# Performance work log

Hardware: AMD Instinct MI355X
Metric: run time of the kernel (lower is better)

The kernel has to match this reference:

```python
import jax, jax.numpy as jnp
import numpy as np

N = 384          # item_num (text regions)
TD = 768         # text hidden (bert-base)
VD = 768         # vision hidden (vit-base)
CD = TD + VD     # commu_dim = 1536
FF = 2048        # TransformerEncoderLayer default dim_feedforward
H = 4            # nhead
L = 2            # num_layers per encoder
EPS = 1e-5


def _enc_params(key, d, scale=0.02):
    ks = jax.random.split(key, 6)
    return dict(
        qkv_w=jax.random.normal(ks[0], (L, 3 * d, d), jnp.float32) * scale,
        qkv_b=jnp.zeros((L, 3 * d), jnp.float32),
        out_w=jax.random.normal(ks[1], (L, d, d), jnp.float32) * scale,
        out_b=jnp.zeros((L, d), jnp.float32),
        ln1_s=jnp.ones((L, d), jnp.float32),
        ln1_b=jnp.zeros((L, d), jnp.float32),
        ff1_w=jax.random.normal(ks[2], (L, FF, d), jnp.float32) * scale,
        ff1_b=jnp.zeros((L, FF), jnp.float32),
        ff2_w=jax.random.normal(ks[3], (L, d, FF), jnp.float32) * scale,
        ff2_b=jnp.zeros((L, d), jnp.float32),
        ln2_s=jnp.ones((L, d), jnp.float32),
        ln2_b=jnp.zeros((L, d), jnp.float32),
    )


def setup_inputs() -> dict:
    key = jax.random.key(0)
    k = jax.random.split(key, 6)
    inp = {
        'text_emb': jax.random.normal(k[0], (N, TD), jnp.float32),
        'vision_emb': jax.random.normal(k[1], (N, VD), jnp.float32),
        'gt_matrix': jax.random.randint(k[2], (N, N), 0, 2, jnp.int32),
    }
    for pref, kk, d in (('t_', k[3], TD), ('c_', k[4], CD)):
        for name, v in _enc_params(kk, d).items():
            inp[pref + name] = v
    inp['lin_w'] = jax.random.normal(k[5], (2, 2 * CD), jnp.float32) * 0.02
    inp['lin_b'] = jnp.zeros((2,), jnp.float32)
    return inp


def _ln(x, s, b):
    m = jnp.mean(x, -1, keepdims=True)
    v = jnp.mean((x - m) ** 2, -1, keepdims=True)
    return (x - m) * jax.lax.rsqrt(v + EPS) * s + b


def _encoder(x, qkv_w, qkv_b, out_w, out_b, ln1_s, ln1_b,
             ff1_w, ff1_b, ff2_w, ff2_b, ln2_s, ln2_b):
    # PyTorch post-norm TransformerEncoder, relu activation, eval mode (no dropout)
    d = x.shape[-1]
    hd = d // H
    for l in range(qkv_w.shape[0]):
        qkv = x @ qkv_w[l].T + qkv_b[l]
        q, kk, v = jnp.split(qkv, 3, axis=-1)
        q = q.reshape(-1, H, hd)
        kk = kk.reshape(-1, H, hd)
        v = v.reshape(-1, H, hd)
        scores = jnp.einsum('qhd,khd->hqk', q, kk) / jnp.sqrt(jnp.float32(hd))
        attn = jax.nn.softmax(scores, -1)
        o = jnp.einsum('hqk,khd->qhd', attn, v).reshape(-1, d)
        x = _ln(x + o @ out_w[l].T + out_b[l], ln1_s[l], ln1_b[l])
        h = jax.nn.relu(x @ ff1_w[l].T + ff1_b[l]) @ ff2_w[l].T + ff2_b[l]
        x = _ln(x + h, ln2_s[l], ln2_b[l])
    return x


def reference(text_emb, vision_emb, gt_matrix,
              t_qkv_w, t_qkv_b, t_out_w, t_out_b, t_ln1_s, t_ln1_b,
              t_ff1_w, t_ff1_b, t_ff2_w, t_ff2_b, t_ln2_s, t_ln2_b,
              c_qkv_w, c_qkv_b, c_out_w, c_out_b, c_ln1_s, c_ln1_b,
              c_ff1_w, c_ff1_b, c_ff2_w, c_ff2_b, c_ln2_s, c_ln2_b,
              lin_w, lin_b):
    te = _encoder(text_emb, t_qkv_w, t_qkv_b, t_out_w, t_out_b, t_ln1_s, t_ln1_b,
                  t_ff1_w, t_ff1_b, t_ff2_w, t_ff2_b, t_ln2_s, t_ln2_b)
    all_emb = jnp.concatenate([te, vision_emb], axis=1)  # [N, CD]
    all_emb = _encoder(all_emb, c_qkv_w, c_qkv_b, c_out_w, c_out_b, c_ln1_s, c_ln1_b,
                       c_ff1_w, c_ff1_b, c_ff2_w, c_ff2_b, c_ln2_s, c_ln2_b)
    # organize(): linear(cat(e_i, e_j)) decomposes exactly as e_i@Wa^T + e_j@Wb^T + b,
    # avoiding the O(N^2 * 2*CD) pair tensor while computing identical math.
    a = all_emb @ lin_w[:, :CD].T + lin_b      # [N, 2]
    c = all_emb @ lin_w[:, CD:].T              # [N, 2]
    logits = a[:, None, :] + c[None, :, :]     # [N, N, 2]
    probs = jax.nn.softmax(logits, -1)         # self.activate(self.linear(...))
    # classificaiton_loss: sum_i CrossEntropyLoss(probs[i], gt[i])  (CE takes probs as logits)
    ls = jax.nn.log_softmax(probs, -1)
    cell = -jnp.take_along_axis(ls, gt_matrix[..., None].astype(jnp.int32), axis=-1)[..., 0]
    cls_loss = jnp.sum(jnp.mean(cell, axis=1))
    # enter_exit_loss over first N-1 items
    link = probs[:, :, 1]
    ee_loss = jnp.sum(jnp.abs(link.sum(1)[:-1] + link.sum(0)[:-1] - 1.0))
    return probs, cls_loss, ee_loss
```

## Files before the change

kernel.cpp:

```cpp
#include <hip/hip_runtime.h>
#include <hip/hip_bf16.h>
#include <math.h>

#define NTOK 384
#define HEADS 4

typedef __attribute__((ext_vector_type(8))) short bf16x8;
typedef __attribute__((ext_vector_type(4))) float f32x4;

__device__ __forceinline__ unsigned short f2b(float f) {
    union { float f; unsigned int u; } v; v.f = f;
    unsigned int r = (v.u + 0x7fff + ((v.u >> 16) & 1)) >> 16;
    return (unsigned short)r;
}

__device__ __forceinline__ void g2l16(const void* g, void* l) {
    __builtin_amdgcn_global_load_lds(
        (const __attribute__((address_space(1))) unsigned int*)g,
        (__attribute__((address_space(3))) unsigned int*)l, 16, 0, 0);
}

__device__ __forceinline__ void stage64(
    const unsigned short* __restrict__ g, int row0, int k0, int ld,
    char* region, int wid, int lane)
{
    int c = wid * 64 + lane;
    int row = c >> 2, p = c & 3;
    int kc = (p - (row >> 1)) & 3;
    g2l16(g + (long)(row0 + row) * ld + k0 + kc * 8,
          region + (wid * 64) * 16);
}

__device__ __forceinline__ void stage_tile(
    const unsigned short* __restrict__ A, const unsigned short* __restrict__ B,
    int row0, int col0, int k0, int lda, int ldb,
    char* buf, int wid, int lane)
{
    stage64(A, row0, k0,      lda, buf,         wid, lane);
    stage64(A, row0, k0 + 32, lda, buf +  4096, wid, lane);
    stage64(B, col0, k0,      ldb, buf +  8192, wid, lane);
    stage64(B, col0, k0 + 32, ldb, buf + 12288, wid, lane);
    __builtin_amdgcn_sched_barrier(0);
}

__global__ __launch_bounds__(256, 3) void gemm64(
    const unsigned short* __restrict__ A, const unsigned short* __restrict__ B,
    const float* __restrict__ bias, void* __restrict__ Cv,
    int K, int lda, int ldb, int ldc,
    long sA, long sB, long sC, int relu, int out_bf16,
    unsigned short* __restrict__ vt, int dv2)
{
    __shared__ char smem[3][16384];
    A += (long)blockIdx.z * sA;
    B += (long)blockIdx.z * sB;
    const int t = threadIdx.x, lane = t & 63, wid = t >> 6;
    const int wm = wid >> 1, wn = wid & 1;
    const int r16 = lane & 15, quad = lane >> 4;
    const int row0 = blockIdx.y * 64, col0 = blockIdx.x * 64;

    f32x4 acc[2][2] = {};
    const int NT = K >> 6;

    stage_tile(A, B, row0, col0, 0, lda, ldb, smem[0], wid, lane);
    if (NT > 1)
        stage_tile(A, B, row0, col0, 64, lda, ldb, smem[1], wid, lane);

    int cur = 0, sb = 2;
    for (int kt = 0; kt < NT; ++kt) {
        if (kt + 1 < NT) asm volatile("s_waitcnt vmcnt(4)" ::: "memory");
        else             asm volatile("s_waitcnt vmcnt(0) lgkmcnt(0)" ::: "memory");
        __builtin_amdgcn_s_barrier();
        if (kt + 2 < NT) {
            stage_tile(A, B, row0, col0, (kt + 2) * 64, lda, ldb,
                       smem[sb], wid, lane);
            sb = (sb == 2) ? 0 : sb + 1;
        }
        const char* cb = smem[cur];
        cur = (cur == 2) ? 0 : cur + 1;
        #pragma unroll
        for (int h = 0; h < 2; ++h) {
            bf16x8 af[2], bfv[2];
            #pragma unroll
            for (int rt = 0; rt < 2; ++rt) {
                int row = wm * 32 + rt * 16 + r16;
                int p = (quad + (row >> 1)) & 3;
                af[rt] = *reinterpret_cast<const bf16x8*>(
                    cb + h * 4096 + row * 64 + p * 16);
            }
            #pragma unroll
            for (int ct = 0; ct < 2; ++ct) {
                int col = wn * 32 + ct * 16 + r16;
                int p = (quad + (col >> 1)) & 3;
                bfv[ct] = *reinterpret_cast<const bf16x8*>(
                    cb + 8192 + h * 4096 + col * 64 + p * 16);
            }
            #pragma unroll
            for (int rt = 0; rt < 2; ++rt)
                #pragma unroll
                for (int ct = 0; ct < 2; ++ct)
                    acc[rt][ct] = __builtin_amdgcn_mfma_f32_16x16x32_bf16(
                        af[rt], bfv[ct], acc[rt][ct], 0, 0, 0);
        }
    }

    float* Cf = (float*)Cv;
    unsigned short* Cb = (unsigned short*)Cv;
    const long zoff = (long)blockIdx.z * sC;
    const int vwrite = (vt != nullptr) && (col0 >= dv2);
    #pragma unroll
    for (int rt = 0; rt < 2; ++rt) {
        #pragma unroll
        for (int ct = 0; ct < 2; ++ct) {
            f32x4 v = acc[rt][ct];
            int col = col0 + wn * 32 + ct * 16 + r16;
            float bi = bias ? bias[col] : 0.f;
            #pragma unroll
            for (int i = 0; i < 4; ++i) {
                v[i] += bi;
                if (relu) v[i] = fmaxf(v[i], 0.f);
            }
            int rbase = row0 + wm * 32 + rt * 16 + quad * 4;
            if (vwrite) {
                ushort4 p;
                p.x = f2b(v[0]); p.y = f2b(v[1]); p.z = f2b(v[2]); p.w = f2b(v[3]);
                *reinterpret_cast<ushort4*>(vt + (long)(col - dv2) * NTOK + rbase) = p;
            } else if (out_bf16) {
                #pragma unroll
                for (int i = 0; i < 4; ++i)
                    Cb[zoff + (long)(rbase + i) * ldc + col] = f2b(v[i]);
            } else {
                #pragma unroll
                for (int i = 0; i < 4; ++i)
                    Cf[zoff + (long)(rbase + i) * ldc + col] = v[i];
            }
        }
    }
}

#define WO0 0u
#define WO1 3538944u
#define WO2 4718592u
#define WO3 7864320u
#define WO4 11010048u
#define WO5 25165824u
#define WO6 29884416u
#define WO7 36175872u
#define WTOT 42467328u

__global__ __launch_bounds__(256) void convert_weights(
    const float* __restrict__ s0, const float* __restrict__ s1,
    const float* __restrict__ s2, const float* __restrict__ s3,
    const float* __restrict__ s4, const float* __restrict__ s5,
    const float* __restrict__ s6, const float* __restrict__ s7,
    unsigned short* __restrict__ dst)
{
    unsigned int e = (blockIdx.x * 256u + threadIdx.x) * 16u;
    if (e >= WTOT) return;
    const float* src; unsigned int local;
    if      (e < WO1) { src = s0; local = e - WO0; }
    else if (e < WO2) { src = s1; local = e - WO1; }
    else if (e < WO3) { src = s2; local = e - WO2; }
    else if (e < WO4) { src = s3; local = e - WO3; }
    else if (e < WO5) { src = s4; local = e - WO4; }
    else if (e < WO6) { src = s5; local = e - WO5; }
    else if (e < WO7) { src = s6; local = e - WO6; }
    else              { src = s7; local = e - WO7; }
    float4 v0 = *reinterpret_cast<const float4*>(src + local);
    float4 v1 = *reinterpret_cast<const float4*>(src + local + 4);
    float4 v2 = *reinterpret_cast<const float4*>(src + local + 8);
    float4 v3 = *reinterpret_cast<const float4*>(src + local + 12);
    uint4 o0, o1;
    o0.x = (unsigned)f2b(v0.x) | ((unsigned)f2b(v0.y) << 16);
    o0.y = (unsigned)f2b(v0.z) | ((unsigned)f2b(v0.w) << 16);
    o0.z = (unsigned)f2b(v1.x) | ((unsigned)f2b(v1.y) << 16);
    o0.w = (unsigned)f2b(v1.z) | ((unsigned)f2b(v1.w) << 16);
    o1.x = (unsigned)f2b(v2.x) | ((unsigned)f2b(v2.y) << 16);
    o1.y = (unsigned)f2b(v2.z) | ((unsigned)f2b(v2.w) << 16);
    o1.z = (unsigned)f2b(v3.x) | ((unsigned)f2b(v3.y) << 16);
    o1.w = (unsigned)f2b(v3.z) | ((unsigned)f2b(v3.w) << 16);
    *reinterpret_cast<uint4*>(dst + e) = o0;
    *reinterpret_cast<uint4*>(dst + e + 8) = o1;
}

__global__ __launch_bounds__(64) void softmax_rows(
    const float* __restrict__ S, unsigned short* __restrict__ P, float scale)
{
    const float* p = S + (long)blockIdx.x * NTOK;
    unsigned short* q = P + (long)blockIdx.x * NTOK;
    const int t = threadIdx.x;
    float vals[6];
    float vmax = -1e30f;
    #pragma unroll
    for (int i = 0; i < 6; ++i) {
        vals[i] = p[t + i * 64] * scale;
        vmax = fmaxf(vmax, vals[i]);
    }
    for (int off = 32; off; off >>= 1) vmax = fmaxf(vmax, __shfl_down(vmax, off));
    vmax = __shfl(vmax, 0);
    float sum = 0.f;
    #pragma unroll
    for (int i = 0; i < 6; ++i) { vals[i] = __expf(vals[i] - vmax); sum += vals[i]; }
    for (int off = 32; off; off >>= 1) sum += __shfl_down(sum, off);
    sum = __shfl(sum, 0);
    float inv = 1.f / sum;
    #pragma unroll
    for (int i = 0; i < 6; ++i) q[t + i * 64] = f2b(vals[i] * inv);
}

__global__ __launch_bounds__(256) void add_ln(
    float* __restrict__ x, unsigned short* __restrict__ xb,
    const float* __restrict__ y, long ps, int np,
    const float* __restrict__ gb,
    const float* __restrict__ s, const float* __restrict__ b, int d)
{
    float* xr = x + (long)blockIdx.x * d;
    unsigned short* xbr = xb + (long)blockIdx.x * d;
    const float* yr = y + (long)blockIdx.x * d;
    const int t = threadIdx.x;
    float vv[6];
    float s1 = 0.f, s2 = 0.f;
    #pragma unroll
    for (int j = 0; j < 6; ++j) {
        int i = t + j * 256;
        if (j * 256 < d) {
            float v = xr[i] + gb[i];
            for (int p = 0; p < np; ++p) v += yr[i + p * ps];
            vv[j] = v;
            s1 += v; s2 += v * v;
        }
    }
    for (int off = 32; off; off >>= 1) { s1 += __shfl_down(s1, off); s2 += __shfl_down(s2, off); }
    __shared__ float r1[4], r2[4];
    int w = t >> 6;
    if ((t & 63) == 0) { r1[w] = s1; r2[w] = s2; }
    __syncthreads();
    if (t == 0) {
        float a = 0.f, c = 0.f;
        for (int i = 0; i < 4; ++i) { a += r1[i]; c += r2[i]; }
        r1[0] = a; r2[0] = c;
    }
    __syncthreads();
    float mean = r1[0] / d;
    float var = r2[0] / d - mean * mean;
    float rstd = rsqrtf(var + 1e-5f);
    #pragma unroll
    for (int j = 0; j < 6; ++j) {
        int i = t + j * 256;
        if (j * 256 < d) {
            float v = (vv[j] - mean) * rstd * s[i] + b[i];
            xr[i] = v;
            xbr[i] = f2b(v);
        }
    }
}

__global__ void initx_k(const float* __restrict__ src, float* __restrict__ dst,
                        unsigned short* __restrict__ dstb, int n)
{
    int i = blockIdx.x * blockDim.x + threadIdx.x;
    if (i < n) { float v = src[i]; dst[i] = v; dstb[i] = f2b(v); }
}

__global__ void concat_k(const float* __restrict__ te, const float* __restrict__ ve,
                         float* __restrict__ all, unsigned short* __restrict__ allb)
{
    int i = blockIdx.x * blockDim.x + threadIdx.x;
    if (i >= NTOK * 1536) return;
    int r = i / 1536, c = i % 1536;
    float v = (c < 768) ? te[r * 768 + c] : ve[r * 768 + (c - 768)];
    all[i] = v;
    allb[i] = f2b(v);
}

__global__ __launch_bounds__(256) void head_ac(
    const float* __restrict__ all, const float* __restrict__ lin_w,
    const float* __restrict__ lin_b, float* __restrict__ a, float* __restrict__ c)
{
    const int i = blockIdx.x, t = threadIdx.x;
    const float* xr = all + (long)i * 1536;
    float s0 = 0.f, s1 = 0.f, s2 = 0.f, s3 = 0.f;
    for (int e = t; e < 1536; e += 256) {
        float v = xr[e];
        s0 += v * lin_w[e];
        s1 += v * lin_w[3072 + e];
        s2 += v * lin_w[1536 + e];
        s3 += v * lin_w[4608 + e];
    }
    for (int off = 32; off; off >>= 1) {
        s0 += __shfl_down(s0, off); s1 += __shfl_down(s1, off);
        s2 += __shfl_down(s2, off); s3 += __shfl_down(s3, off);
    }
    __shared__ float r[4][4];
    int w = t >> 6;
    if ((t & 63) == 0) { r[0][w] = s0; r[1][w] = s1; r[2][w] = s2; r[3][w] = s3; }
    __syncthreads();
    if (t == 0) {
        float t0 = 0.f, t1 = 0.f, t2 = 0.f, t3 = 0.f;
        for (int k = 0; k < 4; ++k) { t0 += r[0][k]; t1 += r[1][k]; t2 += r[2][k]; t3 += r[3][k]; }
        a[i * 2 + 0] = t0 + lin_b[0];
        a[i * 2 + 1] = t1 + lin_b[1];
        c[i * 2 + 0] = t2;
        c[i * 2 + 1] = t3;
    }
}

__global__ __launch_bounds__(384) void head_probs(
    const float* __restrict__ a, const float* __restrict__ c,
    const int* __restrict__ gt, float* __restrict__ probs,
    float* __restrict__ rowsum, float* __restrict__ rowcell)
{
    const int i = blockIdx.x, j = threadIdx.x;
    float l0 = a[i * 2 + 0] + c[j * 2 + 0];
    float l1 = a[i * 2 + 1] + c[j * 2 + 1];
    float m = fmaxf(l0, l1);
    float e0 = __expf(l0 - m), e1 = __expf(l1 - m);
    float inv = 1.f / (e0 + e1);
    float p0 = e0 * inv, p1 = e1 * inv;
    long base = ((long)i * NTOK + j) * 2;
    probs[base] = p0;
    probs[base + 1] = p1;
    float m2 = fmaxf(p0, p1);
    float z = m2 + __logf(__expf(p0 - m2) + __expf(p1 - m2));
    int g = gt[i * NTOK + j];
    float cell = z - (g ? p1 : p0);
    float cs = cell, ps = p1;
    for (int off = 32; off; off >>= 1) { cs += __shfl_down(cs, off); ps += __shfl_down(ps, off); }
    __shared__ float rc[6], rs[6];
    int w = j >> 6;
    if ((j & 63) == 0) { rc[w] = cs; rs[w] = ps; }
    __syncthreads();
    if (j == 0) {
        float csum = 0.f, psum = 0.f;
        for (int k = 0; k < 6; ++k) { csum += rc[k]; psum += rs[k]; }
        rowcell[i] = csum * (1.f / NTOK);
        rowsum[i] = psum;
    }
}

__global__ __launch_bounds__(64) void colsum_k(const float* __restrict__ probs,
                                               float* __restrict__ colsum)
{
    const int j = blockIdx.x, t = threadIdx.x;
    float s = 0.f;
    for (int i = t; i < NTOK; i += 64)
        s += probs[((long)i * NTOK + j) * 2 + 1];
    for (int off = 32; off; off >>= 1) s += __shfl_down(s, off);
    if (t == 0) colsum[j] = s;
}

__global__ __launch_bounds__(384) void finalize_k(
    const float* __restrict__ rowcell, const float* __restrict__ rowsum,
    const float* __restrict__ colsum, float* __restrict__ out)
{
    const int t = threadIdx.x;
    float cls = rowcell[t];
    float ee = (t < NTOK - 1) ? fabsf(rowsum[t] + colsum[t] - 1.f) : 0.f;
    for (int off = 32; off; off >>= 1) { cls += __shfl_down(cls, off); ee += __shfl_down(ee, off); }
    __shared__ float rc[6], re[6];
    int w = t >> 6;
    if ((t & 63) == 0) { rc[w] = cls; re[w] = ee; }
    __syncthreads();
    if (t == 0) {
        float a = 0.f, b = 0.f;
        for (int k = 0; k < 6; ++k) { a += rc[k]; b += re[k]; }
        out[NTOK * NTOK * 2 + 0] = a;
        out[NTOK * NTOK * 2 + 1] = b;
    }
}

static void run_encoder(float* x, unsigned short* xb, int d,
                        const unsigned short* wq, const unsigned short* wo,
                        const unsigned short* w1, const unsigned short* w2,
                        const float* qkv_b, const float* out_b,
                        const float* ln1_s, const float* ln1_b,
                        const float* ff1_b, const float* ff2_b,
                        const float* ln2_s, const float* ln2_b,
                        unsigned short* qkvb, float* sc, unsigned short* attnb,
                        unsigned short* vtb, unsigned short* ob,
                        unsigned short* t1b, float* t2,
                        hipStream_t stream)
{
    const int dq = 3 * d;
    const int hd = d / HEADS;
    const float scale = 1.0f / sqrtf((float)hd);
    const int np_out = (d == 768) ? 2 : 3;
    const int ks_out = d / np_out;
    const int np_ff2 = 4, ks_ff2 = 512;
    const long psC = (long)NTOK * d;
    for (int l = 0; l < 2; ++l) {
        gemm64<<<dim3(dq / 64, 6), 256, 0, stream>>>(
            xb, wq + (long)l * dq * d, qkv_b + l * dq, qkvb,
            d, d, d, dq, 0, 0, 0, 0, 1, vtb, 2 * d);
        gemm64<<<dim3(6, 6, HEADS), 256, 0, stream>>>(
            qkvb, qkvb + d, nullptr, sc,
            hd, dq, dq, NTOK, (long)hd, (long)hd, (long)NTOK * NTOK,
            0, 0, nullptr, 0);
        softmax_rows<<<HEADS * NTOK, 64, 0, stream>>>(sc, attnb, scale);
        gemm64<<<dim3(hd / 64, 6, HEADS), 256, 0, stream>>>(
            attnb, vtb, nullptr, ob,
            NTOK, NTOK, NTOK, d, (long)NTOK * NTOK, (long)hd * NTOK, (long)hd,
            0, 1, nullptr, 0);
        gemm64<<<dim3(d / 64, 6, np_out), 256, 0, stream>>>(
            ob, wo + (long)l * d * d, nullptr, t2,
            ks_out, d, d, d, (long)ks_out, (long)ks_out, psC, 0, 0, nullptr, 0);
        add_ln<<<NTOK, 256, 0, stream>>>(x, xb, t2, psC, np_out,
                                         out_b + l * d, ln1_s + l * d, ln1_b + l * d, d);
        gemm64<<<dim3(2048 / 64, 6), 256, 0, stream>>>(
            xb, w1 + (long)l * 2048 * d, ff1_b + l * 2048, t1b,
            d, d, d, 2048, 0, 0, 0, 1, 1, nullptr, 0);
        gemm64<<<dim3(d / 64, 6, np_ff2), 256, 0, stream>>>(
            t1b, w2 + (long)l * d * 2048, nullptr, t2,
            ks_ff2, 2048, 2048, d, (long)ks_ff2, (long)ks_ff2, psC, 0, 0, nullptr, 0);
        add_ln<<<NTOK, 256, 0, stream>>>(x, xb, t2, psC, np_ff2,
                                         ff2_b + l * d, ln2_s + l * d, ln2_b + l * d, d);
    }
}

extern "C" void kernel_launch(void* const* d_in, const int* in_sizes, int n_in,
                              void* d_out, int out_size, void* d_ws, size_t ws_size,
                              hipStream_t stream)
{
    const float* text_emb   = (const float*)d_in[0];
    const float* vision_emb = (const float*)d_in[1];
    const int*   gt         = (const int*)  d_in[2];
    const float* t_qkv_w = (const float*)d_in[3];
    const float* t_qkv_b = (const float*)d_in[4];
    const float* t_out_w = (const float*)d_in[5];
    const float* t_out_b = (const float*)d_in[6];
    const float* t_ln1_s = (const float*)d_in[7];
    const float* t_ln1_b = (const float*)d_in[8];
    const float* t_ff1_w = (const float*)d_in[9];
    const float* t_ff1_b = (const float*)d_in[10];
    const float* t_ff2_w = (const float*)d_in[11];
    const float* t_ff2_b = (const float*)d_in[12];
    const float* t_ln2_s = (const float*)d_in[13];
    const float* t_ln2_b = (const float*)d_in[14];
    const float* c_qkv_w = (const float*)d_in[15];
    const float* c_qkv_b = (const float*)d_in[16];
    const float* c_out_w = (const float*)d_in[17];
    const float* c_out_b = (const float*)d_in[18];
    const float* c_ln1_s = (const float*)d_in[19];
    const float* c_ln1_b = (const float*)d_in[20];
    const float* c_ff1_w = (const float*)d_in[21];
    const float* c_ff1_b = (const float*)d_in[22];
    const float* c_ff2_w = (const float*)d_in[23];
    const float* c_ff2_b = (const float*)d_in[24];
    const float* c_ln2_s = (const float*)d_in[25];
    const float* c_ln2_b = (const float*)d_in[26];
    const float* lin_w   = (const float*)d_in[27];
    const float* lin_b   = (const float*)d_in[28];
    float* out = (float*)d_out;

    float* ws = (float*)d_ws;
    float* xt      = ws;
    float* all     = xt + 294912;
    float* t2      = all + 589824;
    float* sc      = t2 + 2359296;
    float* abuf    = sc + 589824;
    float* cbuf    = abuf + 768;
    float* rowsum  = cbuf + 768;
    float* rowcell = rowsum + 384;
    float* colsum  = rowcell + 384;
    unsigned short* ub = (unsigned short*)(ws + 3836544);
    unsigned short* xtb   = ub;
    unsigned short* allb  = xtb + 294912;
    unsigned short* qkvb  = allb + 589824;
    unsigned short* attnb = qkvb + 1769472;
    unsigned short* vtb   = attnb + 589824;
    unsigned short* ob    = vtb + 589824;
    unsigned short* t1b   = ob + 589824;
    unsigned short* wb    = t1b + 786432;

    convert_weights<<<(WTOT / 16 + 255) / 256, 256, 0, stream>>>(
        t_qkv_w, t_out_w, t_ff1_w, t_ff2_w,
        c_qkv_w, c_out_w, c_ff1_w, c_ff2_w, wb);

    initx_k<<<(294912 + 255) / 256, 256, 0, stream>>>(text_emb, xt, xtb, 294912);
    run_encoder(xt, xtb, 768,
                wb + WO0, wb + WO1, wb + WO2, wb + WO3,
                t_qkv_b, t_out_b, t_ln1_s, t_ln1_b,
                t_ff1_b, t_ff2_b, t_ln2_s, t_ln2_b,
                qkvb, sc, attnb, vtb, ob, t1b, t2, stream);

    concat_k<<<(589824 + 255) / 256, 256, 0, stream>>>(xt, vision_emb, all, allb);
    run_encoder(all, allb, 1536,
                wb + WO4, wb + WO5, wb + WO6, wb + WO7,
                c_qkv_b, c_out_b, c_ln1_s, c_ln1_b,
                c_ff1_b, c_ff2_b, c_ln2_s, c_ln2_b,
                qkvb, sc, attnb, vtb, ob, t1b, t2, stream);

    head_ac<<<NTOK, 256, 0, stream>>>(all, lin_w, lin_b, abuf, cbuf);
    head_probs<<<NTOK, 384, 0, stream>>>(abuf, cbuf, gt, out, rowsum, rowcell);
    colsum_k<<<NTOK, 64, 0, stream>>>(out, colsum);
    finalize_k<<<1, 384, 0, stream>>>(rowcell, rowsum, colsum, out);
}
```

Measured before the change: 514.4 us.

## Use 128x128 GEMM tiles for projections and drop split-K partial sums

Adds a 512-thread gemm128 kernel with 128x128 output tiles and uses it for the QKV, output-projection, FF1 and FF2 GEMMs. The output-projection and FF2 GEMMs no longer split K into partial slabs, so add_ln reads a single result instead of summing partials, and the workspace layout shrinks to match. Larger tiles raise per-block data reuse and cut partial-sum traffic, but they launch far fewer blocks (for example 6x3 for the d=768 projections), which can leave most of the GPU's compute units idle and make each block run the full K loop.

```diff
diff --git a/kernel.cpp b/kernel.cpp
--- a/kernel.cpp
+++ b/kernel.cpp
@@ -47,8 +47,7 @@
     const unsigned short* __restrict__ A, const unsigned short* __restrict__ B,
     const float* __restrict__ bias, void* __restrict__ Cv,
     int K, int lda, int ldb, int ldc,
-    long sA, long sB, long sC, int relu, int out_bf16,
-    unsigned short* __restrict__ vt, int dv2)
+    long sA, long sB, long sC, int relu, int out_bf16)
 {
     __shared__ char smem[3][16384];
     A += (long)blockIdx.z * sA;
@@ -106,7 +105,6 @@
     float* Cf = (float*)Cv;
     unsigned short* Cb = (unsigned short*)Cv;
     const long zoff = (long)blockIdx.z * sC;
-    const int vwrite = (vt != nullptr) && (col0 >= dv2);
     #pragma unroll
     for (int rt = 0; rt < 2; ++rt) {
         #pragma unroll
@@ -120,6 +118,114 @@
                 if (relu) v[i] = fmaxf(v[i], 0.f);
             }
             int rbase = row0 + wm * 32 + rt * 16 + quad * 4;
+            if (out_bf16) {
+                #pragma unroll
+                for (int i = 0; i < 4; ++i)
+                    Cb[zoff + (long)(rbase + i) * ldc + col] = f2b(v[i]);
+            } else {
+                #pragma unroll
+                for (int i = 0; i < 4; ++i)
+                    Cf[zoff + (long)(rbase + i) * ldc + col] = v[i];
+            }
+        }
+    }
+}
+
+__device__ __forceinline__ void stage128(
+    const unsigned short* __restrict__ g, int row0, int k0, int ld,
+    char* region, int tid)
+{
+    int row = tid >> 2, p = tid & 3;
+    int kc = (p - (row >> 1)) & 3;
+    g2l16(g + (long)(row0 + row) * ld + k0 + kc * 8,
+          region + ((tid >> 6) * 64) * 16);
+}
+
+__device__ __forceinline__ void stage_tile128(
+    const unsigned short* __restrict__ A, const unsigned short* __restrict__ B,
+    int row0, int col0, int k0, int lda, int ldb,
+    char* buf, int tid)
+{
+    stage128(A, row0, k0,      lda, buf,          tid);
+    stage128(A, row0, k0 + 32, lda, buf +  8192,  tid);
+    stage128(B, col0, k0,      ldb, buf + 16384,  tid);
+    stage128(B, col0, k0 + 32, ldb, buf + 24576,  tid);
+    __builtin_amdgcn_sched_barrier(0);
+}
+
+__global__ __launch_bounds__(512, 1) void gemm128(
+    const unsigned short* __restrict__ A, const unsigned short* __restrict__ B,
+    const float* __restrict__ bias, void* __restrict__ Cv,
+    int K, int lda, int ldb, int ldc, int relu, int out_bf16,
+    unsigned short* __restrict__ vt, int dv2)
+{
+    __shared__ char smem[3][32768];
+    const int t = threadIdx.x, lane = t & 63, wid = t >> 6;
+    const int wm = wid >> 2, wn = wid & 3;
+    const int r16 = lane & 15, quad = lane >> 4;
+    const int row0 = blockIdx.y * 128, col0 = blockIdx.x * 128;
+
+    f32x4 acc[4][2] = {};
+    const int NT = K >> 6;
+
+    stage_tile128(A, B, row0, col0, 0, lda, ldb, smem[0], t);
+    if (NT > 1)
+        stage_tile128(A, B, row0, col0, 64, lda, ldb, smem[1], t);
+
+    int cur = 0, sb = 2;
+    for (int kt = 0; kt < NT; ++kt) {
+        if (kt + 1 < NT) asm volatile("s_waitcnt vmcnt(4)" ::: "memory");
+        else             asm volatile("s_waitcnt vmcnt(0) lgkmcnt(0)" ::: "memory");
+        __builtin_amdgcn_s_barrier();
+        if (kt + 2 < NT) {
+            stage_tile128(A, B, row0, col0, (kt + 2) * 64, lda, ldb,
+                          smem[sb], t);
+            sb = (sb == 2) ? 0 : sb + 1;
+        }
+        const char* cb = smem[cur];
+        cur = (cur == 2) ? 0 : cur + 1;
+        #pragma unroll
+        for (int h = 0; h < 2; ++h) {
+            bf16x8 af[4], bfv[2];
+            #pragma unroll
+            for (int rt = 0; rt < 4; ++rt) {
+                int row = wm * 64 + rt * 16 + r16;
+                int p = (quad + (row >> 1)) & 3;
+                af[rt] = *reinterpret_cast<const bf16x8*>(
+                    cb + h * 8192 + row * 64 + p * 16);
+            }
+            #pragma unroll
+            for (int ct = 0; ct < 2; ++ct) {
+                int col = wn * 32 + ct * 16 + r16;
+                int p = (quad + (col >> 1)) & 3;
+                bfv[ct] = *reinterpret_cast<const bf16x8*>(
+                    cb + 16384 + h * 8192 + col * 64 + p * 16);
+            }
+            #pragma unroll
+            for (int rt = 0; rt < 4; ++rt)
+                #pragma unroll
+                for (int ct = 0; ct < 2; ++ct)
+                    acc[rt][ct] = __builtin_amdgcn_mfma_f32_16x16x32_bf16(
+                        af[rt], bfv[ct], acc[rt][ct], 0, 0, 0);
+        }
+    }
+
+    float* Cf = (float*)Cv;
+    unsigned short* Cb = (unsigned short*)Cv;
+    const int vwrite = (vt != nullptr) && (col0 >= dv2);
+    #pragma unroll
+    for (int rt = 0; rt < 4; ++rt) {
+        #pragma unroll
+        for (int ct = 0; ct < 2; ++ct) {
+            f32x4 v = acc[rt][ct];
+            int col = col0 + wn * 32 + ct * 16 + r16;
+            float bi = bias ? bias[col] : 0.f;
+            #pragma unroll
+            for (int i = 0; i < 4; ++i) {
+                v[i] += bi;
+                if (relu) v[i] = fmaxf(v[i], 0.f);
+            }
+            int rbase = row0 + wm * 64 + rt * 16 + quad * 4;
             if (vwrite) {
                 ushort4 p;
                 p.x = f2b(v[0]); p.y = f2b(v[1]); p.z = f2b(v[2]); p.w = f2b(v[3]);
@@ -127,11 +233,11 @@
             } else if (out_bf16) {
                 #pragma unroll
                 for (int i = 0; i < 4; ++i)
-                    Cb[zoff + (long)(rbase + i) * ldc + col] = f2b(v[i]);
+                    Cb[(long)(rbase + i) * ldc + col] = f2b(v[i]);
             } else {
                 #pragma unroll
                 for (int i = 0; i < 4; ++i)
-                    Cf[zoff + (long)(rbase + i) * ldc + col] = v[i];
+                    Cf[(long)(rbase + i) * ldc + col] = v[i];
             }
         }
     }
@@ -209,7 +315,7 @@
 
 __global__ __launch_bounds__(256) void add_ln(
     float* __restrict__ x, unsigned short* __restrict__ xb,
-    const float* __restrict__ y, long ps, int np,
+    const float* __restrict__ y,
     const float* __restrict__ gb,
     const float* __restrict__ s, const float* __restrict__ b, int d)
 {
@@ -223,8 +329,7 @@
     for (int j = 0; j < 6; ++j) {
         int i = t + j * 256;
         if (j * 256 < d) {
-            float v = xr[i] + gb[i];
-            for (int p = 0; p < np; ++p) v += yr[i + p * ps];
+            float v = xr[i] + gb[i] + yr[i];
             vv[j] = v;
             s1 += v; s2 += v * v;
         }
@@ -383,35 +488,30 @@
     const int dq = 3 * d;
     const int hd = d / HEADS;
     const float scale = 1.0f / sqrtf((float)hd);
-    const int np_out = (d == 768) ? 2 : 3;
-    const int ks_out = d / np_out;
-    const int np_ff2 = 4, ks_ff2 = 512;
-    const long psC = (long)NTOK * d;
     for (int l = 0; l < 2; ++l) {
-        gemm64<<<dim3(dq / 64, 6), 256, 0, stream>>>(
+        gemm128<<<dim3(dq / 128, NTOK / 128), 512, 0, stream>>>(
             xb, wq + (long)l * dq * d, qkv_b + l * dq, qkvb,
-            d, d, d, dq, 0, 0, 0, 0, 1, vtb, 2 * d);
+            d, d, d, dq, 0, 1, vtb, 2 * d);
         gemm64<<<dim3(6, 6, HEADS), 256, 0, stream>>>(
             qkvb, qkvb + d, nullptr, sc,
-            hd, dq, dq, NTOK, (long)hd, (long)hd, (long)NTOK * NTOK,
-            0, 0, nullptr, 0);
+            hd, dq, dq, NTOK, (long)hd, (long)hd, (long)NTOK * NTOK, 0, 0);
         softmax_rows<<<HEADS * NTOK, 64, 0, stream>>>(sc, attnb, scale);
         gemm64<<<dim3(hd / 64, 6, HEADS), 256, 0, stream>>>(
             attnb, vtb, nullptr, ob,
             NTOK, NTOK, NTOK, d, (long)NTOK * NTOK, (long)hd * NTOK, (long)hd,
-            0, 1, nullptr, 0);
-        gemm64<<<dim3(d / 64, 6, np_out), 256, 0, stream>>>(
+            0, 1);
+        gemm128<<<dim3(d / 128, NTOK / 128), 512, 0, stream>>>(
             ob, wo + (long)l * d * d, nullptr, t2,
-            ks_out, d, d, d, (long)ks_out, (long)ks_out, psC, 0, 0, nullptr, 0);
-        add_ln<<<NTOK, 256, 0, stream>>>(x, xb, t2, psC, np_out,
+            d, d, d, d, 0, 0, nullptr, 0);
+        add_ln<<<NTOK, 256, 0, stream>>>(x, xb, t2,
                                          out_b + l * d, ln1_s + l * d, ln1_b + l * d, d);
-        gemm64<<<dim3(2048 / 64, 6), 256, 0, stream>>>(
+        gemm128<<<dim3(2048 / 128, NTOK / 128), 512, 0, stream>>>(
             xb, w1 + (long)l * 2048 * d, ff1_b + l * 2048, t1b,
-            d, d, d, 2048, 0, 0, 0, 1, 1, nullptr, 0);
-        gemm64<<<dim3(d / 64, 6, np_ff2), 256, 0, stream>>>(
+            d, d, d, 2048, 1, 1, nullptr, 0);
+        gemm128<<<dim3(d / 128, NTOK / 128), 512, 0, stream>>>(
             t1b, w2 + (long)l * d * 2048, nullptr, t2,
-            ks_ff2, 2048, 2048, d, (long)ks_ff2, (long)ks_ff2, psC, 0, 0, nullptr, 0);
-        add_ln<<<NTOK, 256, 0, stream>>>(x, xb, t2, psC, np_ff2,
+            2048, 2048, 2048, d, 0, 0, nullptr, 0);
+        add_ln<<<NTOK, 256, 0, stream>>>(x, xb, t2,
                                          ff2_b + l * d, ln2_s + l * d, ln2_b + l * d, d);
     }
 }
@@ -455,13 +555,13 @@
     float* xt      = ws;
     float* all     = xt + 294912;
     float* t2      = all + 589824;
-    float* sc      = t2 + 2359296;
+    float* sc      = t2 + 589824;
     float* abuf    = sc + 589824;
     float* cbuf    = abuf + 768;
     float* rowsum  = cbuf + 768;
     float* rowcell = rowsum + 384;
     float* colsum  = rowcell + 384;
-    unsigned short* ub = (unsigned short*)(ws + 3836544);
+    unsigned short* ub = (unsigned short*)(ws + 2067072);
     unsigned short* xtb   = ub;
     unsigned short* allb  = xtb + 294912;
     unsigned short* qkvb  = allb + 589824;
```

Result: slower. 607.8 us (+18.1%).
